# Performance work log

Measured on AMD Instinct MI355X. Metric: run time of the kernel, lower is better.

Reference implementation:

```python
import jax, jax.numpy as jnp
import numpy as np

B, T, IN = 32, 1024, 256
H = 128          # hidden_size
NL = 2           # num_layers
NC = 4           # num_classes
F2 = 2 * H       # bidirectional feature size


def _lstm_dir(xs, w_ih, w_hh, b_ih, b_hh, reverse):
    # xs: [T, B, in]; w_ih: [4H, in]; w_hh: [4H, H]
    if reverse:
        xs = xs[::-1]
    h0 = jnp.zeros((xs.shape[1], H), xs.dtype)
    c0 = jnp.zeros((xs.shape[1], H), xs.dtype)

    def step(carry, xt):
        h, c = carry
        g = xt @ w_ih.T + b_ih + h @ w_hh.T + b_hh  # [B, 4H]
        i, f, gg, o = jnp.split(g, 4, axis=-1)       # PyTorch gate order i,f,g,o
        c = jax.nn.sigmoid(f) * c + jax.nn.sigmoid(i) * jnp.tanh(gg)
        h = jax.nn.sigmoid(o) * jnp.tanh(c)
        return (h, c), h

    _, hs = jax.lax.scan(step, (h0, c0), xs)  # [T, B, H]
    if reverse:
        hs = hs[::-1]
    return hs


def setup_inputs() -> dict:
    key = jax.random.key(0)
    ks = jax.random.split(key, 12)
    s = 0.05
    x = jax.random.normal(ks[0], (B, T, IN), jnp.float32)
    # stacked LSTM params: [layer, direction, ...]; layer0 in = IN, layer1 in = 2H = IN
    w_ih = jax.random.normal(ks[1], (NL, 2, 4 * H, IN), jnp.float32) * s
    w_hh = jax.random.normal(ks[2], (NL, 2, 4 * H, H), jnp.float32) * s
    b_ih = jax.random.normal(ks[3], (NL, 2, 4 * H), jnp.float32) * s
    b_hh = jax.random.normal(ks[4], (NL, 2, 4 * H), jnp.float32) * s
    wq = jax.random.normal(ks[5], (F2, F2), jnp.float32) * s
    wk = jax.random.normal(ks[6], (F2, F2), jnp.float32) * s
    wv = jax.random.normal(ks[7], (F2, F2), jnp.float32) * s
    bq = jax.random.normal(ks[8], (F2,), jnp.float32) * s
    bk = jax.random.normal(ks[9], (F2,), jnp.float32) * s
    bv = jax.random.normal(ks[10], (F2,), jnp.float32) * s
    w_fc = jax.random.normal(ks[11], (NC, F2), jnp.float32) * s
    b_fc = jnp.zeros((NC,), jnp.float32)
    return {"x": x, "w_ih": w_ih, "w_hh": w_hh, "b_ih": b_ih, "b_hh": b_hh,
            "wq": wq, "wk": wk, "wv": wv, "bq": bq, "bk": bk, "bv": bv,
            "w_fc": w_fc, "b_fc": b_fc}


def reference(x, w_ih, w_hh, b_ih, b_hh, wq, wk, wv, bq, bk, bv, w_fc, b_fc):
    # --- biLSTM (eval mode: inter-layer dropout inactive) ---
    xs = jnp.swapaxes(x, 0, 1)  # time-major [T, B, IN]
    for l in range(NL):
        fwd = _lstm_dir(xs, w_ih[l, 0], w_hh[l, 0], b_ih[l, 0], b_hh[l, 0], False)
        bwd = _lstm_dir(xs, w_ih[l, 1], w_hh[l, 1], b_ih[l, 1], b_hh[l, 1], True)
        xs = jnp.concatenate([fwd, bwd], axis=-1)  # [T, B, 2H]
    out = jnp.swapaxes(xs, 0, 1)  # [B, T, 2H]
    # --- naive full self-attention ---
    q = out @ wq.T + bq
    k = out @ wk.T + bk
    v = out @ wv.T + bv
    scores = jnp.einsum('btd,bsd->bts', q, k) / jnp.sqrt(jnp.float32(F2))
    attn = jax.nn.softmax(scores, axis=-1)          # [B, T, T]
    ctx = jnp.einsum('bts,bsd->btd', attn, v)       # [B, T, 2H]
    # --- FC head on last timestep ---
    return ctx[:, -1, :] @ w_fc.T + b_fc            # [B, NC]
```

## Files before the change

kernel.cpp:

```cpp
#include <hip/hip_runtime.h>
#include <math.h>
#include <stdint.h>

#define BB 32
#define TT 1024
#define HH 128
#define G4 512
#define CH 16
#define XPS 516

typedef _Float16 half2_t __attribute__((ext_vector_type(2)));
typedef _Float16 half8_t __attribute__((ext_vector_type(8)));
typedef float f32x4 __attribute__((ext_vector_type(4)));
typedef __attribute__((address_space(3))) uint32_t lds_u32;
typedef __attribute__((address_space(1))) const uint32_t glb_u32;

__device__ __forceinline__ float fdot2f(half2_t a, half2_t b, float c) {
    return __builtin_amdgcn_fdot2(a, b, c, false);
}
__device__ __forceinline__ float rcpf(float x) {
    return __builtin_amdgcn_rcpf(x);
}
__device__ __forceinline__ float dpp_xor1(float x) {
    return __builtin_bit_cast(float, __builtin_amdgcn_update_dpp(
        0, __builtin_bit_cast(int, x), 0xB1, 0xF, 0xF, true));
}
__device__ __forceinline__ float dpp_xor2(float x) {
    return __builtin_bit_cast(float, __builtin_amdgcn_update_dpp(
        0, __builtin_bit_cast(int, x), 0x4E, 0xF, 0xF, true));
}
__device__ __forceinline__ void bar_lgkm() {
    asm volatile("s_waitcnt lgkmcnt(0)\n\ts_barrier" ::: "memory");
}

__global__ __launch_bounds__(256) void cvt_wih(
    const float* __restrict__ w, _Float16* __restrict__ o)
{
    const int i = (blockIdx.x * 256 + threadIdx.x) * 4;
    float4 f = *(const float4*)(w + i);
    half2_t t[2] = { half2_t{(_Float16)f.x, (_Float16)f.y},
                     half2_t{(_Float16)f.z, (_Float16)f.w} };
    *(float2*)(o + i) = *(float2*)t;
}

__global__ __attribute__((amdgpu_waves_per_eu(2, 2))) __launch_bounds__(512)
void lstm_fused(
    const float* __restrict__ x_in,
    const _Float16* __restrict__ wih16_l,
    const float* __restrict__ b_ih_l,
    const float* __restrict__ b_hh_l,
    const float* __restrict__ w_hh_l,
    float* __restrict__ out)
{
    const int b = blockIdx.x & 31;
    const int d = blockIdx.x >> 5;
    const int tid = threadIdx.x;
    const int wvid = tid >> 6;
    const int l = tid & 63;
    const int s = l & 3;
    const int g = l >> 2;
    const int j = (wvid << 4) | g;

    __shared__ __align__(16) _Float16 hs[HH];
    __shared__ __align__(16) float xp[2][CH * XPS];
    __shared__ __align__(16) half2_t xr[2][CH * 128];
    __shared__ __align__(16) float obuf[CH * HH];
    __shared__ __align__(16) float xstage[CH * 256];

    half2_t wv[4][16];
#pragma unroll
    for (int G = 0; G < 4; ++G) {
        const float* wr = w_hh_l + (size_t)(d * G4 + 128 * G + j) * HH + 32 * s;
#pragma unroll
        for (int q4 = 0; q4 < 8; ++q4) {
            float4 f = *(const float4*)(wr + 4 * q4);
            wv[G][2 * q4]     = half2_t{(_Float16)f.x, (_Float16)f.y};
            wv[G][2 * q4 + 1] = half2_t{(_Float16)f.z, (_Float16)f.w};
        }
    }

    const int acol0 = wvid * 64 + (l & 15);
    const _Float16* wn = wih16_l + ((size_t)d * G4 + acol0) * 256 + (l >> 4) * 8;
    const float bias0 = b_ih_l[d * G4 + acol0]      + b_hh_l[d * G4 + acol0];
    const float bias1 = b_ih_l[d * G4 + acol0 + 16] + b_hh_l[d * G4 + acol0 + 16];
    const float bias2 = b_ih_l[d * G4 + acol0 + 32] + b_hh_l[d * G4 + acol0 + 32];
    const float bias3 = b_ih_l[d * G4 + acol0 + 48] + b_hh_l[d * G4 + acol0 + 48];

    half8_t wf0[8], wf1[8], wf2[8], wf3[8];
#pragma unroll
    for (int kt = 0; kt < 8; ++kt) {
        wf0[kt] = *(const half8_t*)(wn +         kt * 32);
        wf1[kt] = *(const half8_t*)(wn +  4096 + kt * 32);
        wf2[kt] = *(const half8_t*)(wn +  8192 + kt * 32);
        wf3[kt] = *(const half8_t*)(wn + 12288 + kt * 32);
    }

    const int cbase = ((acol0 & 127) << 2) + (acol0 >> 7);

    const float* xbase = x_in + (size_t)b * TT * 256;

    const int a_noswz = (l & 15) * 512 + (l >> 4) * 16;
    const int a_swz   = (l & 7) << 4;
    const int w_swz_byte = (tid * 16) ^ (((tid >> 5) & 7) << 4);

#pragma unroll 1
    for (int p = 0; p < 2; ++p) {
        const int tlo = d ? (1008 - p * CH) : p * CH;
        const float* gs = xbase + (size_t)tlo * 256 + tid * 8;
        float4 f0 = *(const float4*)gs;
        float4 f1 = *(const float4*)(gs + 4);
        half2_t t4[4] = { half2_t{(_Float16)f0.x, (_Float16)f0.y},
                          half2_t{(_Float16)f0.z, (_Float16)f0.w},
                          half2_t{(_Float16)f1.x, (_Float16)f1.y},
                          half2_t{(_Float16)f1.z, (_Float16)f1.w} };
        *(float4*)((char*)xr[p] + w_swz_byte) = *(float4*)t4;
    }
    __syncthreads();

    f32x4 acc0 = {bias0, bias0, bias0, bias0};
    f32x4 acc1 = {bias1, bias1, bias1, bias1};
    f32x4 acc2 = {bias2, bias2, bias2, bias2};
    f32x4 acc3 = {bias3, bias3, bias3, bias3};

#pragma unroll
    for (int kt = 0; kt < 8; ++kt) {
        half8_t af = *(const half8_t*)((const char*)xr[0] + ((a_noswz + kt * 64) ^ a_swz));
        acc0 = __builtin_amdgcn_mfma_f32_16x16x32_f16(af, wf0[kt], acc0, 0, 0, 0);
        acc1 = __builtin_amdgcn_mfma_f32_16x16x32_f16(af, wf1[kt], acc1, 0, 0, 0);
        acc2 = __builtin_amdgcn_mfma_f32_16x16x32_f16(af, wf2[kt], acc2, 0, 0, 0);
        acc3 = __builtin_amdgcn_mfma_f32_16x16x32_f16(af, wf3[kt], acc3, 0, 0, 0);
    }
    {
        const int rb = (l >> 4) * 4;
#pragma unroll
        for (int q = 0; q < 4; ++q) {
            const int ix = (rb + q) * XPS + cbase;
            xp[0][ix]       = acc0[q];
            xp[0][ix + 64]  = acc1[q];
            xp[0][ix + 128] = acc2[q];
            xp[0][ix + 192] = acc3[q];
        }
    }
    acc0 = (f32x4){bias0, bias0, bias0, bias0};
    acc1 = (f32x4){bias1, bias1, bias1, bias1};
    acc2 = (f32x4){bias2, bias2, bias2, bias2};
    acc3 = (f32x4){bias3, bias3, bias3, bias3};

    if (tid < 64) ((half2_t*)hs)[tid] = half2_t{(_Float16)0.f, (_Float16)0.f};
    float c = 0.f;
    float* ob = out + (size_t)b * TT * 256 + d * HH;
    __syncthreads();

    for (int ck = 0; ck < 64; ++ck) {
        const int cur = ck & 1;
        const bool doproj = (ck + 1 < 64);
        if (ck + 2 < 64) {
            const int tlo2 = d ? (1008 - (ck + 2) * CH) : (ck + 2) * CH;
            const float* gsrc = xbase + (size_t)tlo2 * 256;
#pragma unroll
            for (int cc = 0; cc < 2; ++cc)
                __builtin_amdgcn_global_load_lds(
                    (glb_u32*)(gsrc + tid * 4 + cc * 2048),
                    (lds_u32*)&xstage[tid * 4 + cc * 2048],
                    16, 0, 0);
        }
        const float* xb = xp[cur];
        const char* xr_rd = (const char*)xr[cur ^ 1];

        auto rec_step = [&](int si) {
            const int lds_t = d ? (CH - 1 - si) : si;
            const float4 xg4 = *(const float4*)&xb[lds_t * XPS + (j << 2)];

            const float4* hp = (const float4*)(hs + 32 * s);
            float4 hA = hp[0], hB = hp[1], hC = hp[2], hD = hp[3];
            half2_t hh[16];
            hh[0]  = __builtin_bit_cast(half2_t, hA.x);
            hh[1]  = __builtin_bit_cast(half2_t, hA.y);
            hh[2]  = __builtin_bit_cast(half2_t, hA.z);
            hh[3]  = __builtin_bit_cast(half2_t, hA.w);
            hh[4]  = __builtin_bit_cast(half2_t, hB.x);
            hh[5]  = __builtin_bit_cast(half2_t, hB.y);
            hh[6]  = __builtin_bit_cast(half2_t, hB.z);
            hh[7]  = __builtin_bit_cast(half2_t, hB.w);
            hh[8]  = __builtin_bit_cast(half2_t, hC.x);
            hh[9]  = __builtin_bit_cast(half2_t, hC.y);
            hh[10] = __builtin_bit_cast(half2_t, hC.z);
            hh[11] = __builtin_bit_cast(half2_t, hC.w);
            hh[12] = __builtin_bit_cast(half2_t, hD.x);
            hh[13] = __builtin_bit_cast(half2_t, hD.y);
            hh[14] = __builtin_bit_cast(half2_t, hD.z);
            hh[15] = __builtin_bit_cast(half2_t, hD.w);

            float a0 = 0.f, a1 = 0.f, a2 = 0.f, a3 = 0.f;
            float e0 = 0.f, e1 = 0.f, e2 = 0.f, e3 = 0.f;
#pragma unroll
            for (int kk = 0; kk < 8; ++kk) {
                a0 = fdot2f(wv[0][kk], hh[kk], a0);
                a1 = fdot2f(wv[1][kk], hh[kk], a1);
                a2 = fdot2f(wv[2][kk], hh[kk], a2);
                a3 = fdot2f(wv[3][kk], hh[kk], a3);
                e0 = fdot2f(wv[0][kk + 8], hh[kk + 8], e0);
                e1 = fdot2f(wv[1][kk + 8], hh[kk + 8], e1);
                e2 = fdot2f(wv[2][kk + 8], hh[kk + 8], e2);
                e3 = fdot2f(wv[3][kk + 8], hh[kk + 8], e3);
            }
            a0 += e0; a1 += e1; a2 += e2; a3 += e3;

            a0 += dpp_xor1(a0); a0 += dpp_xor2(a0);
            a1 += dpp_xor1(a1); a1 += dpp_xor2(a1);
            a2 += dpp_xor1(a2); a2 += dpp_xor2(a2);
            a3 += dpp_xor1(a3); a3 += dpp_xor2(a3);

            const float gi = rcpf(1.f + __expf(-(a0 + xg4.x)));
            const float gf = rcpf(1.f + __expf(-(a1 + xg4.y)));
            const float gg = 1.f - 2.f * rcpf(1.f + __expf(2.f * (a2 + xg4.z)));
            const float go = rcpf(1.f + __expf(-(a3 + xg4.w)));
            c = gf * c + gi * gg;
            const float th = 1.f - 2.f * rcpf(1.f + __expf(2.f * c));
            const float h = go * th;
            if (s == 0) {
                hs[j] = (_Float16)h;
                obuf[si * HH + j] = h;
            }
        };

#pragma unroll
        for (int sp = 0; sp < CH / 2; ++sp) {
            half8_t afrag = {};
            if (doproj)
                afrag = *(const half8_t*)(xr_rd + ((a_noswz + sp * 64) ^ a_swz));
            rec_step(2 * sp);
            if (doproj) {
                acc0 = __builtin_amdgcn_mfma_f32_16x16x32_f16(afrag, wf0[sp], acc0, 0, 0, 0);
                acc1 = __builtin_amdgcn_mfma_f32_16x16x32_f16(afrag, wf1[sp], acc1, 0, 0, 0);
            }
            bar_lgkm();
            rec_step(2 * sp + 1);
            if (doproj) {
                acc2 = __builtin_amdgcn_mfma_f32_16x16x32_f16(afrag, wf2[sp], acc2, 0, 0, 0);
                acc3 = __builtin_amdgcn_mfma_f32_16x16x32_f16(afrag, wf3[sp], acc3, 0, 0, 0);
            }
            bar_lgkm();
        }

        {
            const int idx = tid * 4;
            const int sf = idx >> 7, jf = idx & 127;
            const int sg = ck * CH + sf;
            const int t  = d ? (TT - 1 - sg) : sg;
            float4 o0 = *(const float4*)&obuf[idx];
            *(float4*)&ob[(size_t)t * 256 + jf] = o0;
        }
        if (doproj) {
            float* xpn = xp[cur ^ 1];
            const int rb = (l >> 4) * 4;
#pragma unroll
            for (int q = 0; q < 4; ++q) {
                const int ix = (rb + q) * XPS + cbase;
                xpn[ix]       = acc0[q];
                xpn[ix + 64]  = acc1[q];
                xpn[ix + 128] = acc2[q];
                xpn[ix + 192] = acc3[q];
            }
            acc0 = (f32x4){bias0, bias0, bias0, bias0};
            acc1 = (f32x4){bias1, bias1, bias1, bias1};
            acc2 = (f32x4){bias2, bias2, bias2, bias2};
            acc3 = (f32x4){bias3, bias3, bias3, bias3};
        }
        if (ck + 2 < 64) {
            asm volatile("s_waitcnt vmcnt(0)" ::: "memory");
            float4 f0 = *(const float4*)&xstage[tid * 8];
            float4 f1 = *(const float4*)&xstage[tid * 8 + 4];
            half2_t t4[4] = { half2_t{(_Float16)f0.x, (_Float16)f0.y},
                              half2_t{(_Float16)f0.z, (_Float16)f0.w},
                              half2_t{(_Float16)f1.x, (_Float16)f1.y},
                              half2_t{(_Float16)f1.z, (_Float16)f1.w} };
            *(float4*)((char*)xr[cur] + w_swz_byte) = *(float4*)t4;
        }
        __syncthreads();
    }
}

__global__ __launch_bounds__(1024) void attn_kernel(
    const float* __restrict__ out1,
    const float* __restrict__ wq, const float* __restrict__ bq,
    const float* __restrict__ wk,
    const float* __restrict__ wv, const float* __restrict__ bv,
    const float* __restrict__ wfc, const float* __restrict__ bfc,
    float* __restrict__ outp)
{
    const int b = blockIdx.x;
    const int tid = threadIdx.x;
    const int n = tid & 255, qq = tid >> 8;

    __shared__ float xl[256], q[256], u[256], cx[256];
    __shared__ __align__(16) float r[256];
    __shared__ float sc[TT];
    __shared__ float red[1024];
    __shared__ float part[4][256];

    const float* ob = out1 + (size_t)b * TT * 256;

    if (tid < 256) xl[tid] = ob[(size_t)(TT - 1) * 256 + tid];
    __syncthreads();

    {
        float a = 0.f;
        const float* wr = wq + (size_t)n * 256 + qq * 64;
        const float* xq = xl + qq * 64;
#pragma unroll 8
        for (int k = 0; k < 64; ++k) a += xq[k] * wr[k];
        part[qq][n] = a;
    }
    __syncthreads();
    if (tid < 256) q[tid] = bq[tid] + part[0][tid] + part[1][tid] + part[2][tid] + part[3][tid];
    __syncthreads();

    {
        float a = 0.f;
        const float* wkp = wk + (size_t)(qq * 64) * 256 + n;
#pragma unroll 8
        for (int dd = 0; dd < 64; ++dd) a += q[qq * 64 + dd] * wkp[(size_t)dd * 256];
        part[qq][n] = a;
    }
    __syncthreads();
    if (tid < 256) r[tid] = part[0][tid] + part[1][tid] + part[2][tid] + part[3][tid];
    __syncthreads();

    {
        const int wave = tid >> 6, lane = tid & 63;
        float4 r4 = *(const float4*)&r[lane * 4];
        for (int t = wave; t < TT; t += 16) {
            float4 o4 = *(const float4*)(ob + (size_t)t * 256 + lane * 4);
            float p = r4.x * o4.x + r4.y * o4.y + r4.z * o4.z + r4.w * o4.w;
#pragma unroll
            for (int off = 32; off > 0; off >>= 1) p += __shfl_down(p, off, 64);
            if (lane == 0) sc[t] = p * 0.0625f;
        }
    }
    __syncthreads();

    float v = sc[tid];
    red[tid] = v; __syncthreads();
    for (int st = 512; st > 0; st >>= 1) {
        if (tid < st) red[tid] = fmaxf(red[tid], red[tid + st]);
        __syncthreads();
    }
    const float mx = red[0]; __syncthreads();
    const float e = expf(v - mx);
    sc[tid] = e;
    red[tid] = e; __syncthreads();
    for (int st = 512; st > 0; st >>= 1) {
        if (tid < st) red[tid] += red[tid + st];
        __syncthreads();
    }
    const float inv = 1.f / red[0];
    __syncthreads();

    {
        float a = 0.f;
        const float* op = ob + (size_t)(qq * 256) * 256 + n;
        const float* sp = sc + qq * 256;
#pragma unroll 4
        for (int t = 0; t < 256; ++t) a += sp[t] * op[(size_t)t * 256];
        part[qq][n] = a;
    }
    __syncthreads();
    if (tid < 256) u[tid] = (part[0][tid] + part[1][tid] + part[2][tid] + part[3][tid]) * inv;
    __syncthreads();

    {
        float a = 0.f;
        const float* wr = wv + (size_t)n * 256 + qq * 64;
#pragma unroll 8
        for (int k = 0; k < 64; ++k) a += u[qq * 64 + k] * wr[k];
        part[qq][n] = a;
    }
    __syncthreads();
    if (tid < 256) cx[tid] = bv[tid] + part[0][tid] + part[1][tid] + part[2][tid] + part[3][tid];
    __syncthreads();

    if (tid < 4) {
        float o = bfc[tid];
        for (int k = 0; k < 256; ++k) o += cx[k] * wfc[tid * 256 + k];
        outp[b * 4 + tid] = o;
    }
}

extern "C" void kernel_launch(void* const* d_in, const int* in_sizes, int n_in,
                              void* d_out, int out_size, void* d_ws, size_t ws_size,
                              hipStream_t stream)
{
    const float* x    = (const float*)d_in[0];
    const float* w_ih = (const float*)d_in[1];
    const float* w_hh = (const float*)d_in[2];
    const float* b_ih = (const float*)d_in[3];
    const float* b_hh = (const float*)d_in[4];
    const float* wq   = (const float*)d_in[5];
    const float* wk   = (const float*)d_in[6];
    const float* wv   = (const float*)d_in[7];
    const float* bq   = (const float*)d_in[8];
    const float* bv   = (const float*)d_in[10];
    const float* wfc  = (const float*)d_in[11];
    const float* bfcv = (const float*)d_in[12];
    float* outp = (float*)d_out;

    float* ws = (float*)d_ws;
    _Float16* wih16 = (_Float16*)ws;
    float* out0 = ws + 262144;
    float* out1 = out0 + 8388608;

    cvt_wih<<<512, 256, 0, stream>>>(w_ih, wih16);

    lstm_fused<<<64, 512, 0, stream>>>(x, wih16, b_ih, b_hh, w_hh, out0);
    lstm_fused<<<64, 512, 0, stream>>>(out0, wih16 + 262144, b_ih + 1024, b_hh + 1024,
                                       w_hh + 2 * 512 * 128, out1);
    attn_kernel<<<32, 1024, 0, stream>>>(out1, wq, bq, wk, wv, bv, wfc, bfcv, outp);
}
```

Baseline: 1.763 ms.

## Halve LSTM block to 256 threads, each thread computing two hidden units

Shrinks the fused LSTM block from 8 waves to 4 so that each thread owns two hidden units, with twice the recurrent weights and twice the MFMA input-projection accumulators held in registers. The per-step barriers then synchronise fewer waves, which should cut barrier latency on the sequential recurrence. The cost is doubled register pressure (waves_per_eu set to 1) and twice the serial work per thread on each timestep, which may outweigh the cheaper barriers.

```diff
diff --git a/kernel.cpp b/kernel.cpp
--- a/kernel.cpp
+++ b/kernel.cpp
@@ -43,7 +43,7 @@
     *(float2*)(o + i) = *(float2*)t;
 }
 
-__global__ __attribute__((amdgpu_waves_per_eu(2, 2))) __launch_bounds__(512)
+__global__ __attribute__((amdgpu_waves_per_eu(1, 1))) __launch_bounds__(256)
 void lstm_fused(
     const float* __restrict__ x_in,
     const _Float16* __restrict__ wih16_l,
@@ -58,8 +58,8 @@
     const int wvid = tid >> 6;
     const int l = tid & 63;
     const int s = l & 3;
-    const int g = l >> 2;
-    const int j = (wvid << 4) | g;
+    const int q = (wvid << 4) | (l >> 2);
+    const int j0 = q << 1;
 
     __shared__ __align__(16) _Float16 hs[HH];
     __shared__ __align__(16) float xp[2][CH * XPS];
@@ -67,90 +67,90 @@
     __shared__ __align__(16) float obuf[CH * HH];
     __shared__ __align__(16) float xstage[CH * 256];
 
-    half2_t wv[4][16];
+    half2_t wv[2][4][16];
+#pragma unroll
+    for (int jj = 0; jj < 2; ++jj)
 #pragma unroll
     for (int G = 0; G < 4; ++G) {
-        const float* wr = w_hh_l + (size_t)(d * G4 + 128 * G + j) * HH + 32 * s;
+        const float* wr = w_hh_l + (size_t)(d * G4 + 128 * G + j0 + jj) * HH + 32 * s;
 #pragma unroll
         for (int q4 = 0; q4 < 8; ++q4) {
             float4 f = *(const float4*)(wr + 4 * q4);
-            wv[G][2 * q4]     = half2_t{(_Float16)f.x, (_Float16)f.y};
-            wv[G][2 * q4 + 1] = half2_t{(_Float16)f.z, (_Float16)f.w};
-        }
-    }
-
-    const int acol0 = wvid * 64 + (l & 15);
+            wv[jj][G][2 * q4]     = half2_t{(_Float16)f.x, (_Float16)f.y};
+            wv[jj][G][2 * q4 + 1] = half2_t{(_Float16)f.z, (_Float16)f.w};
+        }
+    }
+
+    const int acol0 = (wvid << 7) + (l & 15);
     const _Float16* wn = wih16_l + ((size_t)d * G4 + acol0) * 256 + (l >> 4) * 8;
-    const float bias0 = b_ih_l[d * G4 + acol0]      + b_hh_l[d * G4 + acol0];
-    const float bias1 = b_ih_l[d * G4 + acol0 + 16] + b_hh_l[d * G4 + acol0 + 16];
-    const float bias2 = b_ih_l[d * G4 + acol0 + 32] + b_hh_l[d * G4 + acol0 + 32];
-    const float bias3 = b_ih_l[d * G4 + acol0 + 48] + b_hh_l[d * G4 + acol0 + 48];
-
-    half8_t wf0[8], wf1[8], wf2[8], wf3[8];
-#pragma unroll
-    for (int kt = 0; kt < 8; ++kt) {
-        wf0[kt] = *(const half8_t*)(wn +         kt * 32);
-        wf1[kt] = *(const half8_t*)(wn +  4096 + kt * 32);
-        wf2[kt] = *(const half8_t*)(wn +  8192 + kt * 32);
-        wf3[kt] = *(const half8_t*)(wn + 12288 + kt * 32);
-    }
-
-    const int cbase = ((acol0 & 127) << 2) + (acol0 >> 7);
+    float bias[8];
+    int cix[8];
+#pragma unroll
+    for (int m = 0; m < 8; ++m) {
+        const int n = acol0 + 16 * m;
+        bias[m] = b_ih_l[d * G4 + n] + b_hh_l[d * G4 + n];
+        cix[m] = ((n & 127) << 2) + (n >> 7);
+    }
+
+    half8_t wf[8][8];
+#pragma unroll
+    for (int m = 0; m < 8; ++m)
+#pragma unroll
+    for (int kt = 0; kt < 8; ++kt)
+        wf[m][kt] = *(const half8_t*)(wn + m * 4096 + kt * 32);
 
     const float* xbase = x_in + (size_t)b * TT * 256;
 
     const int a_noswz = (l & 15) * 512 + (l >> 4) * 16;
     const int a_swz   = (l & 7) << 4;
-    const int w_swz_byte = (tid * 16) ^ (((tid >> 5) & 7) << 4);
+    const int cw_swz  = ((tid >> 4) & 7) << 4;
 
 #pragma unroll 1
     for (int p = 0; p < 2; ++p) {
         const int tlo = d ? (1008 - p * CH) : p * CH;
-        const float* gs = xbase + (size_t)tlo * 256 + tid * 8;
-        float4 f0 = *(const float4*)gs;
-        float4 f1 = *(const float4*)(gs + 4);
-        half2_t t4[4] = { half2_t{(_Float16)f0.x, (_Float16)f0.y},
-                          half2_t{(_Float16)f0.z, (_Float16)f0.w},
-                          half2_t{(_Float16)f1.x, (_Float16)f1.y},
-                          half2_t{(_Float16)f1.z, (_Float16)f1.w} };
-        *(float4*)((char*)xr[p] + w_swz_byte) = *(float4*)t4;
-    }
-    __syncthreads();
-
-    f32x4 acc0 = {bias0, bias0, bias0, bias0};
-    f32x4 acc1 = {bias1, bias1, bias1, bias1};
-    f32x4 acc2 = {bias2, bias2, bias2, bias2};
-    f32x4 acc3 = {bias3, bias3, bias3, bias3};
+        const float* gs = xbase + (size_t)tlo * 256 + tid * 16;
+        float4 f[4];
+#pragma unroll
+        for (int i = 0; i < 4; ++i) f[i] = *(const float4*)(gs + 4 * i);
+        half2_t t8[8];
+#pragma unroll
+        for (int i = 0; i < 4; ++i) {
+            t8[2 * i]     = half2_t{(_Float16)f[i].x, (_Float16)f[i].y};
+            t8[2 * i + 1] = half2_t{(_Float16)f[i].z, (_Float16)f[i].w};
+        }
+        *(float4*)((char*)xr[p] + ((tid * 32) ^ cw_swz))      = *(float4*)&t8[0];
+        *(float4*)((char*)xr[p] + ((tid * 32 + 16) ^ cw_swz)) = *(float4*)&t8[4];
+    }
+    __syncthreads();
+
+    f32x4 acc[8];
+#pragma unroll
+    for (int m = 0; m < 8; ++m) acc[m] = (f32x4){bias[m], bias[m], bias[m], bias[m]};
 
 #pragma unroll
     for (int kt = 0; kt < 8; ++kt) {
         half8_t af = *(const half8_t*)((const char*)xr[0] + ((a_noswz + kt * 64) ^ a_swz));
-        acc0 = __builtin_amdgcn_mfma_f32_16x16x32_f16(af, wf0[kt], acc0, 0, 0, 0);
-        acc1 = __builtin_amdgcn_mfma_f32_16x16x32_f16(af, wf1[kt], acc1, 0, 0, 0);
-        acc2 = __builtin_amdgcn_mfma_f32_16x16x32_f16(af, wf2[kt], acc2, 0, 0, 0);
-        acc3 = __builtin_amdgcn_mfma_f32_16x16x32_f16(af, wf3[kt], acc3, 0, 0, 0);
+#pragma unroll
+        for (int m = 0; m < 8; ++m)
+            acc[m] = __builtin_amdgcn_mfma_f32_16x16x32_f16(af, wf[m][kt], acc[m], 0, 0, 0);
     }
     {
         const int rb = (l >> 4) * 4;
 #pragma unroll
-        for (int q = 0; q < 4; ++q) {
-            const int ix = (rb + q) * XPS + cbase;
-            xp[0][ix]       = acc0[q];
-            xp[0][ix + 64]  = acc1[q];
-            xp[0][ix + 128] = acc2[q];
-            xp[0][ix + 192] = acc3[q];
-        }
-    }
-    acc0 = (f32x4){bias0, bias0, bias0, bias0};
-    acc1 = (f32x4){bias1, bias1, bias1, bias1};
-    acc2 = (f32x4){bias2, bias2, bias2, bias2};
-    acc3 = (f32x4){bias3, bias3, bias3, bias3};
+        for (int m = 0; m < 8; ++m)
+#pragma unroll
+        for (int qq = 0; qq < 4; ++qq)
+            xp[0][(rb + qq) * XPS + cix[m]] = acc[m][qq];
+    }
+#pragma unroll
+    for (int m = 0; m < 8; ++m) acc[m] = (f32x4){bias[m], bias[m], bias[m], bias[m]};
 
     if (tid < 64) ((half2_t*)hs)[tid] = half2_t{(_Float16)0.f, (_Float16)0.f};
-    float c = 0.f;
+    float c0 = 0.f, c1 = 0.f;
     float* ob = out + (size_t)b * TT * 256 + d * HH;
     __syncthreads();
 
+#pragma unroll 1
     for (int ck = 0; ck < 64; ++ck) {
         const int cur = ck & 1;
         const bool doproj = (ck + 1 < 64);
@@ -158,10 +158,10 @@
             const int tlo2 = d ? (1008 - (ck + 2) * CH) : (ck + 2) * CH;
             const float* gsrc = xbase + (size_t)tlo2 * 256;
 #pragma unroll
-            for (int cc = 0; cc < 2; ++cc)
+            for (int cc = 0; cc < 4; ++cc)
                 __builtin_amdgcn_global_load_lds(
-                    (glb_u32*)(gsrc + tid * 4 + cc * 2048),
-                    (lds_u32*)&xstage[tid * 4 + cc * 2048],
+                    (glb_u32*)(gsrc + tid * 4 + cc * 1024),
+                    (lds_u32*)&xstage[tid * 4 + cc * 1024],
                     16, 0, 0);
         }
         const float* xb = xp[cur];
@@ -169,7 +169,8 @@
 
         auto rec_step = [&](int si) {
             const int lds_t = d ? (CH - 1 - si) : si;
-            const float4 xg4 = *(const float4*)&xb[lds_t * XPS + (j << 2)];
+            const float4 xgA = *(const float4*)&xb[lds_t * XPS + (j0 << 2)];
+            const float4 xgB = *(const float4*)&xb[lds_t * XPS + (j0 << 2) + 4];
 
             const float4* hp = (const float4*)(hs + 32 * s);
             float4 hA = hp[0], hB = hp[1], hC = hp[2], hD = hp[3];
@@ -191,36 +192,46 @@
             hh[14] = __builtin_bit_cast(half2_t, hD.z);
             hh[15] = __builtin_bit_cast(half2_t, hD.w);
 
-            float a0 = 0.f, a1 = 0.f, a2 = 0.f, a3 = 0.f;
-            float e0 = 0.f, e1 = 0.f, e2 = 0.f, e3 = 0.f;
+            float A[2][4] = {}, E[2][4] = {};
 #pragma unroll
             for (int kk = 0; kk < 8; ++kk) {
-                a0 = fdot2f(wv[0][kk], hh[kk], a0);
-                a1 = fdot2f(wv[1][kk], hh[kk], a1);
-                a2 = fdot2f(wv[2][kk], hh[kk], a2);
-                a3 = fdot2f(wv[3][kk], hh[kk], a3);
-                e0 = fdot2f(wv[0][kk + 8], hh[kk + 8], e0);
-                e1 = fdot2f(wv[1][kk + 8], hh[kk + 8], e1);
-                e2 = fdot2f(wv[2][kk + 8], hh[kk + 8], e2);
-                e3 = fdot2f(wv[3][kk + 8], hh[kk + 8], e3);
-            }
-            a0 += e0; a1 += e1; a2 += e2; a3 += e3;
-
-            a0 += dpp_xor1(a0); a0 += dpp_xor2(a0);
-            a1 += dpp_xor1(a1); a1 += dpp_xor2(a1);
-            a2 += dpp_xor1(a2); a2 += dpp_xor2(a2);
-            a3 += dpp_xor1(a3); a3 += dpp_xor2(a3);
-
-            const float gi = rcpf(1.f + __expf(-(a0 + xg4.x)));
-            const float gf = rcpf(1.f + __expf(-(a1 + xg4.y)));
-            const float gg = 1.f - 2.f * rcpf(1.f + __expf(2.f * (a2 + xg4.z)));
-            const float go = rcpf(1.f + __expf(-(a3 + xg4.w)));
-            c = gf * c + gi * gg;
-            const float th = 1.f - 2.f * rcpf(1.f + __expf(2.f * c));
-            const float h = go * th;
+#pragma unroll
+                for (int jj = 0; jj < 2; ++jj)
+#pragma unroll
+                for (int G = 0; G < 4; ++G) {
+                    A[jj][G] = fdot2f(wv[jj][G][kk],     hh[kk],     A[jj][G]);
+                    E[jj][G] = fdot2f(wv[jj][G][kk + 8], hh[kk + 8], E[jj][G]);
+                }
+            }
+#pragma unroll
+            for (int jj = 0; jj < 2; ++jj)
+#pragma unroll
+            for (int G = 0; G < 4; ++G) {
+                float v = A[jj][G] + E[jj][G];
+                v += dpp_xor1(v); v += dpp_xor2(v);
+                A[jj][G] = v;
+            }
+
+            const float gi0 = rcpf(1.f + __expf(-(A[0][0] + xgA.x)));
+            const float gf0 = rcpf(1.f + __expf(-(A[0][1] + xgA.y)));
+            const float gg0 = 1.f - 2.f * rcpf(1.f + __expf(2.f * (A[0][2] + xgA.z)));
+            const float go0 = rcpf(1.f + __expf(-(A[0][3] + xgA.w)));
+            c0 = gf0 * c0 + gi0 * gg0;
+            const float th0 = 1.f - 2.f * rcpf(1.f + __expf(2.f * c0));
+            const float h0 = go0 * th0;
+
+            const float gi1 = rcpf(1.f + __expf(-(A[1][0] + xgB.x)));
+            const float gf1 = rcpf(1.f + __expf(-(A[1][1] + xgB.y)));
+            const float gg1 = 1.f - 2.f * rcpf(1.f + __expf(2.f * (A[1][2] + xgB.z)));
+            const float go1 = rcpf(1.f + __expf(-(A[1][3] + xgB.w)));
+            c1 = gf1 * c1 + gi1 * gg1;
+            const float th1 = 1.f - 2.f * rcpf(1.f + __expf(2.f * c1));
+            const float h1 = go1 * th1;
+
             if (s == 0) {
-                hs[j] = (_Float16)h;
-                obuf[si * HH + j] = h;
+                ((half2_t*)hs)[q] = half2_t{(_Float16)h0, (_Float16)h1};
+                float2 ov; ov.x = h0; ov.y = h1;
+                *(float2*)&obuf[si * HH + j0] = ov;
             }
         };
 
@@ -231,51 +242,54 @@
                 afrag = *(const half8_t*)(xr_rd + ((a_noswz + sp * 64) ^ a_swz));
             rec_step(2 * sp);
             if (doproj) {
-                acc0 = __builtin_amdgcn_mfma_f32_16x16x32_f16(afrag, wf0[sp], acc0, 0, 0, 0);
-                acc1 = __builtin_amdgcn_mfma_f32_16x16x32_f16(afrag, wf1[sp], acc1, 0, 0, 0);
+#pragma unroll
+                for (int m = 0; m < 4; ++m)
+                    acc[m] = __builtin_amdgcn_mfma_f32_16x16x32_f16(afrag, wf[m][sp], acc[m], 0, 0, 0);
             }
             bar_lgkm();
             rec_step(2 * sp + 1);
             if (doproj) {
-                acc2 = __builtin_amdgcn_mfma_f32_16x16x32_f16(afrag, wf2[sp], acc2, 0, 0, 0);
-                acc3 = __builtin_amdgcn_mfma_f32_16x16x32_f16(afrag, wf3[sp], acc3, 0, 0, 0);
+#pragma unroll
+                for (int m = 4; m < 8; ++m)
+                    acc[m] = __builtin_amdgcn_mfma_f32_16x16x32_f16(afrag, wf[m][sp], acc[m], 0, 0, 0);
             }
             bar_lgkm();
         }
 
         {
-            const int idx = tid * 4;
+            const int idx = tid * 8;
             const int sf = idx >> 7, jf = idx & 127;
             const int sg = ck * CH + sf;
             const int t  = d ? (TT - 1 - sg) : sg;
             float4 o0 = *(const float4*)&obuf[idx];
-            *(float4*)&ob[(size_t)t * 256 + jf] = o0;
+            float4 o1 = *(const float4*)&obuf[idx + 4];
+            *(float4*)&ob[(size_t)t * 256 + jf]     = o0;
+            *(float4*)&ob[(size_t)t * 256 + jf + 4] = o1;
         }
         if (doproj) {
             float* xpn = xp[cur ^ 1];
             const int rb = (l >> 4) * 4;
 #pragma unroll
-            for (int q = 0; q < 4; ++q) {
-                const int ix = (rb + q) * XPS + cbase;
-                xpn[ix]       = acc0[q];
-                xpn[ix + 64]  = acc1[q];
-                xpn[ix + 128] = acc2[q];
-                xpn[ix + 192] = acc3[q];
-            }
-            acc0 = (f32x4){bias0, bias0, bias0, bias0};
-            acc1 = (f32x4){bias1, bias1, bias1, bias1};
-            acc2 = (f32x4){bias2, bias2, bias2, bias2};
-            acc3 = (f32x4){bias3, bias3, bias3, bias3};
+            for (int m = 0; m < 8; ++m)
+#pragma unroll
+            for (int qq = 0; qq < 4; ++qq)
+                xpn[(rb + qq) * XPS + cix[m]] = acc[m][qq];
+#pragma unroll
+            for (int m = 0; m < 8; ++m) acc[m] = (f32x4){bias[m], bias[m], bias[m], bias[m]};
         }
         if (ck + 2 < 64) {
             asm volatile("s_waitcnt vmcnt(0)" ::: "memory");
-            float4 f0 = *(const float4*)&xstage[tid * 8];
-            float4 f1 = *(const float4*)&xstage[tid * 8 + 4];
-            half2_t t4[4] = { half2_t{(_Float16)f0.x, (_Float16)f0.y},
-                              half2_t{(_Float16)f0.z, (_Float16)f0.w},
-                              half2_t{(_Float16)f1.x, (_Float16)f1.y},
-                              half2_t{(_Float16)f1.z, (_Float16)f1.w} };
-            *(float4*)((char*)xr[cur] + w_swz_byte) = *(float4*)t4;
+            float4 f[4];
+#pragma unroll
+            for (int i = 0; i < 4; ++i) f[i] = *(const float4*)&xstage[tid * 16 + 4 * i];
+            half2_t t8[8];
+#pragma unroll
+            for (int i = 0; i < 4; ++i) {
+                t8[2 * i]     = half2_t{(_Float16)f[i].x, (_Float16)f[i].y};
+                t8[2 * i + 1] = half2_t{(_Float16)f[i].z, (_Float16)f[i].w};
+            }
+            *(float4*)((char*)xr[cur] + ((tid * 32) ^ cw_swz))      = *(float4*)&t8[0];
+            *(float4*)((char*)xr[cur] + ((tid * 32 + 16) ^ cw_swz)) = *(float4*)&t8[4];
         }
         __syncthreads();
     }
@@ -412,8 +426,8 @@
 
     cvt_wih<<<512, 256, 0, stream>>>(w_ih, wih16);
 
-    lstm_fused<<<64, 512, 0, stream>>>(x, wih16, b_ih, b_hh, w_hh, out0);
-    lstm_fused<<<64, 512, 0, stream>>>(out0, wih16 + 262144, b_ih + 1024, b_hh + 1024,
+    lstm_fused<<<64, 256, 0, stream>>>(x, wih16, b_ih, b_hh, w_hh, out0);
+    lstm_fused<<<64, 256, 0, stream>>>(out0, wih16 + 262144, b_ih + 1024, b_hh + 1024,
                                        w_hh + 2 * 512 * 128, out1);
     attn_kernel<<<32, 1024, 0, stream>>>(out1, wq, bq, wk, wv, bv, wfc, bfcv, outp);
 }
```

New measurement: 2.352 ms. +33.4%, slower.
